# Kernel tuning notes

Hardware: AMD Instinct MI355X
Metric: run time of the kernel (lower is better)

The kernel has to match this reference:

```python
import jax, jax.numpy as jnp
import numpy as np

N = 4096        # nodes
E = 4096        # hyperedges (source math forces E == N)
B = 3           # behaviors
D_IN = 64
HID = 32
OUT = 32
L = 2           # num_layers
EPS = 1e-6      # DynamicPruningGNN.epsilon
DEG_P = 0.008   # ~32 incidences per node


def setup_inputs() -> dict:
    key = jax.random.key(0)
    ks = jax.random.split(key, 12)
    sc = lambda f: 1.0 / np.sqrt(f)
    X = jax.random.normal(ks[0], (N, D_IN), jnp.float32)
    # sparse binary incidence matrices, stored dense as the original does (H.toarray())
    H = (jax.random.uniform(ks[1], (B, N, E)) < DEG_P).astype(jnp.float32)
    return {
        "X": X,
        "H": H,
        "W_init": jax.random.normal(ks[2], (D_IN, HID), jnp.float32) * sc(D_IN),
        "b_init": jnp.zeros((HID,), jnp.float32),
        "W_node": jax.random.normal(ks[3], (L, HID, HID), jnp.float32) * sc(HID),
        "b_node": jnp.zeros((L, HID), jnp.float32),
        "Theta": jax.random.normal(ks[4], (B, HID, HID), jnp.float32) * sc(HID),
        "behavior_importance": jnp.ones((B,), jnp.float32),
        "Wp1": jax.random.normal(ks[5], (HID, HID), jnp.float32) * sc(HID),
        "bp1": jnp.zeros((HID,), jnp.float32),
        "Wp2": jax.random.normal(ks[6], (HID, OUT), jnp.float32) * sc(HID),
        "bp2": jnp.zeros((OUT,), jnp.float32),
    }


def reference(X, H, W_init, b_init, W_node, b_node, Theta,
              behavior_importance, Wp1, bp1, Wp2, bp2):
    # degree normalizers, clamped like np.maximum(deg, epsilon)
    dv = 1.0 / jnp.sqrt(jnp.maximum(H.sum(axis=2), EPS))   # [B, N]  Dv^-1/2
    de = 1.0 / jnp.maximum(H.sum(axis=1), EPS)             # [B, E]  De^-1
    w = jax.nn.softmax(behavior_importance)                # behavior weights

    x = jax.nn.relu(X @ W_init + b_init)                   # initial_transform  [N, HID]
    for l in range(L):
        xw = x @ W_node[l] + b_node[l]                     # node layer          [N, HID]
        y = dv[:, :, None] * xw[None, :, :]                # Dv^-1/2 . XW       [B, N, HID]
        z = jnp.einsum('bne,bnh->beh', H, y) * de[:, :, None]   # De^-1 H^T ...  [B, E, HID]
        u = jnp.einsum('bne,beh->bnh', H, z) * dv[:, :, None]   # Dv^-1/2 H ...  [B, N, HID]
        msg = jnp.einsum('bnh,bhk->bnk', u, Theta)         # per-behavior Theta [B, N, HID]
        x = jax.nn.relu(jnp.einsum('b,bnk->nk', w, msg))   # weighted multi-behavior agg
    # node_projection: Linear -> ReLU -> Linear
    node_emb = jax.nn.relu(x @ Wp1 + bp1) @ Wp2 + bp2      # [N, OUT]
    return node_emb
```

## Files before the change

kernel.cpp:

```cpp
#include <hip/hip_runtime.h>

#define NN 4096
#define EE 4096
#define BB 3
#define DIN 64
#define HID 32
#define MAXDEG 64
#define EPSF 1e-6f

typedef float nfloat4 __attribute__((ext_vector_type(4)));

__global__ __launch_bounds__(256) void build_all(
        const float* __restrict__ H, const float* __restrict__ X,
        const float* __restrict__ Wi, const float* __restrict__ bi,
        const float* __restrict__ Wn0, const float* __restrict__ bn0,
        int* __restrict__ rowcnt, float* __restrict__ dvinv,
        int* __restrict__ colcnt,
        unsigned short* __restrict__ csr16, unsigned short* __restrict__ csc16,
        float* __restrict__ xw0) {
    __shared__ int el[MAXDEG];
    __shared__ int scnt;
    __shared__ float sh[HID];
    const int bn = blockIdx.x, tid = threadIdx.x;
    const int b = bn >> 12, nrel = bn & (NN - 1);
    if (tid == 0) scnt = 0;
    __syncthreads();
    const nfloat4* row = (const nfloat4*)(H + (size_t)bn * EE);
    nfloat4 v[4];
#pragma unroll
    for (int i = 0; i < 4; i++)
        v[i] = __builtin_nontemporal_load(row + tid + i * 256);
#pragma unroll
    for (int i = 0; i < 4; i++) {
        const nfloat4 w = v[i];
        const int mm = (w.x != 0.f) + (w.y != 0.f) + (w.z != 0.f) + (w.w != 0.f);
        if (mm) {
            int base = atomicAdd(&scnt, mm);
            const int e0 = (tid + i * 256) * 4;
            if (w.x != 0.f) { if (base < MAXDEG) el[base] = e0;     base++; }
            if (w.y != 0.f) { if (base < MAXDEG) el[base] = e0 + 1; base++; }
            if (w.z != 0.f) { if (base < MAXDEG) el[base] = e0 + 2; base++; }
            if (w.w != 0.f) { if (base < MAXDEG) el[base] = e0 + 3; base++; }
        }
    }
    __syncthreads();
    const int cnt = scnt;
    const int m = min(cnt, MAXDEG);
    if (tid == 0) {
        rowcnt[bn] = cnt;
        dvinv[bn] = rsqrtf(fmaxf((float)cnt, EPSF));
    }
    if (tid < MAXDEG)
        csr16[(size_t)bn * MAXDEG + tid] = (tid < m) ? (unsigned short)el[tid] : 0;
    if (tid < m) {
        const int q = (b << 12) + el[tid];
        const int slot = atomicAdd(&colcnt[q], 1);
        if (slot < MAXDEG) csc16[(size_t)q * MAXDEG + slot] = (unsigned short)nrel;
    }
    if (b == 0 && tid < HID) {
        const int h = tid;
        const float* xr = X + (size_t)nrel * DIN;
        float acc = bi[h];
#pragma unroll 8
        for (int d = 0; d < DIN; d++) acc = fmaf(xr[d], Wi[d * HID + h], acc);
        sh[h] = fmaxf(acc, 0.f);
        float a = bn0[h];
#pragma unroll
        for (int k = 0; k < HID; k++) a = fmaf(sh[k], Wn0[k * HID + h], a);
        xw0[nrel * HID + h] = a;
    }
}

__global__ __launch_bounds__(256) void k_z(
        const int* __restrict__ colcnt, const unsigned short* __restrict__ csc16,
        const float* __restrict__ xw, const float* __restrict__ dvinv,
        float* __restrict__ zbuf) {
    const int tid = threadIdx.x, h = tid & 31, g = tid >> 5;
    const int q = blockIdx.x * 8 + g;
    const int cnt = colcnt[q];
    const int m = min(cnt, MAXDEG);
    const int dvbase = q & ~(NN - 1);
    const unsigned int packed = ((const unsigned int*)csc16)[q * 32 + h];
    float acc[8] = {0.f, 0.f, 0.f, 0.f, 0.f, 0.f, 0.f, 0.f};
    for (int j0 = 0; j0 < m; j0 += 8) {
        float vs[8];
#pragma unroll
        for (int k = 0; k < 8; k++) {
            const int j = j0 + k;
            const unsigned int p = __shfl(packed, j >> 1, 32);
            const int id = (j & 1) ? (int)(p >> 16) : (int)(p & 0xffffu);
            vs[k] = xw[id * HID + h] * dvinv[dvbase + id];
        }
#pragma unroll
        for (int k = 0; k < 8; k++) if (j0 + k < m) acc[k] += vs[k];
    }
    const float s = ((acc[0] + acc[1]) + (acc[2] + acc[3]))
                  + ((acc[4] + acc[5]) + (acc[6] + acc[7]));
    zbuf[(size_t)q * HID + h] = s * (1.0f / fmaxf((float)cnt, EPSF));
}

__device__ __forceinline__ float gatherz(const float* __restrict__ zb,
                                         unsigned int packed, int m, int h) {
    float acc[8] = {0.f, 0.f, 0.f, 0.f, 0.f, 0.f, 0.f, 0.f};
    for (int j0 = 0; j0 < m; j0 += 8) {
        float vs[8];
#pragma unroll
        for (int k = 0; k < 8; k++) {
            const int j = j0 + k;
            const unsigned int p = __shfl(packed, j >> 1, 32);
            const int id = (j & 1) ? (int)(p >> 16) : (int)(p & 0xffffu);
            vs[k] = zb[id * HID + h];
        }
#pragma unroll
        for (int k = 0; k < 8; k++) if (j0 + k < m) acc[k] += vs[k];
    }
    return ((acc[0] + acc[1]) + (acc[2] + acc[3]))
         + ((acc[4] + acc[5]) + (acc[6] + acc[7]));
}

__device__ __forceinline__ void softmax3(const float* __restrict__ bimp, float* sw) {
    float b0 = bimp[0], b1 = bimp[1], b2 = bimp[2];
    float mm = fmaxf(b0, fmaxf(b1, b2));
    float e0 = expf(b0 - mm), e1 = expf(b1 - mm), e2 = expf(b2 - mm);
    float s = e0 + e1 + e2;
    sw[0] = e0 / s; sw[1] = e1 / s; sw[2] = e2 / s;
}

__global__ __launch_bounds__(256) void k_layer(
        const float* __restrict__ zbuf,
        const int* __restrict__ rowcnt, const unsigned short* __restrict__ csr16,
        const float* __restrict__ Theta, const float* __restrict__ bimp,
        const float* __restrict__ Wn1, const float* __restrict__ bn1,
        float* __restrict__ xw1) {
    __shared__ float sTh[BB * HID * HID];
    __shared__ float sW[HID * HID];
    __shared__ float sb[HID];
    __shared__ float su[8][HID];
    __shared__ float sw[4];
    const int tid = threadIdx.x;
    for (int i = tid; i < BB * HID * HID; i += 256) sTh[i] = Theta[i];
    for (int i = tid; i < HID * HID; i += 256) sW[i] = Wn1[i];
    if (tid < HID) sb[tid] = bn1[tid];
    if (tid == 0) softmax3(bimp, sw);
    __syncthreads();
    const int h = tid & 31, loc = tid >> 5;
    const int n = blockIdx.x * 8 + loc;
    float accx = 0.f;
#pragma unroll
    for (int b = 0; b < BB; b++) {
        const int r = (b << 12) + n;
        const int cnt = rowcnt[r];
        const int m = min(cnt, MAXDEG);
        const unsigned int packed = ((const unsigned int*)csr16)[r * 32 + h];
        const float u = gatherz(zbuf + (size_t)(b << 12) * HID, packed, m, h)
                        * rsqrtf(fmaxf((float)cnt, EPSF));
        su[loc][h] = u;
        float msg = 0.f;
#pragma unroll
        for (int hh = 0; hh < HID; hh++)
            msg = fmaf(su[loc][hh], sTh[b * (HID * HID) + hh * HID + h], msg);
        accx = fmaf(sw[b], msg, accx);
    }
    su[loc][h] = fmaxf(accx, 0.f);
    float a = sb[h];
#pragma unroll
    for (int hh = 0; hh < HID; hh++) a = fmaf(su[loc][hh], sW[hh * HID + h], a);
    xw1[n * HID + h] = a;
}

__global__ __launch_bounds__(256) void k_final(
        const float* __restrict__ zbuf,
        const int* __restrict__ rowcnt, const unsigned short* __restrict__ csr16,
        const float* __restrict__ Theta, const float* __restrict__ bimp,
        const float* __restrict__ Wp1, const float* __restrict__ bp1,
        const float* __restrict__ Wp2, const float* __restrict__ bp2,
        float* __restrict__ out) {
    __shared__ float sTh[BB * HID * HID];
    __shared__ float sW1[HID * HID], sW2[HID * HID];
    __shared__ float sb1[HID], sb2[HID];
    __shared__ float su[8][HID];
    __shared__ float sw[4];
    const int tid = threadIdx.x;
    for (int i = tid; i < BB * HID * HID; i += 256) sTh[i] = Theta[i];
    for (int i = tid; i < HID * HID; i += 256) { sW1[i] = Wp1[i]; sW2[i] = Wp2[i]; }
    if (tid < HID) { sb1[tid] = bp1[tid]; sb2[tid] = bp2[tid]; }
    if (tid == 0) softmax3(bimp, sw);
    __syncthreads();
    const int h = tid & 31, loc = tid >> 5;
    const int n = blockIdx.x * 8 + loc;
    float accx = 0.f;
#pragma unroll
    for (int b = 0; b < BB; b++) {
        const int r = (b << 12) + n;
        const int cnt = rowcnt[r];
        const int m = min(cnt, MAXDEG);
        const unsigned int packed = ((const unsigned int*)csr16)[r * 32 + h];
        const float u = gatherz(zbuf + (size_t)(b << 12) * HID, packed, m, h)
                        * rsqrtf(fmaxf((float)cnt, EPSF));
        su[loc][h] = u;
        float msg = 0.f;
#pragma unroll
        for (int hh = 0; hh < HID; hh++)
            msg = fmaf(su[loc][hh], sTh[b * (HID * HID) + hh * HID + h], msg);
        accx = fmaf(sw[b], msg, accx);
    }
    su[loc][h] = fmaxf(accx, 0.f);
    float p = sb1[h];
#pragma unroll
    for (int hh = 0; hh < HID; hh++) p = fmaf(su[loc][hh], sW1[hh * HID + h], p);
    su[loc][h] = fmaxf(p, 0.f);
    float o = sb2[h];
#pragma unroll
    for (int hh = 0; hh < HID; hh++) o = fmaf(su[loc][hh], sW2[hh * HID + h], o);
    out[(size_t)n * HID + h] = o;
}

extern "C" void kernel_launch(void* const* d_in, const int* in_sizes, int n_in,
                              void* d_out, int out_size, void* d_ws, size_t ws_size,
                              hipStream_t stream) {
    const float* X      = (const float*)d_in[0];
    const float* H      = (const float*)d_in[1];
    const float* W_init = (const float*)d_in[2];
    const float* b_init = (const float*)d_in[3];
    const float* W_node = (const float*)d_in[4];
    const float* b_node = (const float*)d_in[5];
    const float* Theta  = (const float*)d_in[6];
    const float* bimp   = (const float*)d_in[7];
    const float* Wp1    = (const float*)d_in[8];
    const float* bp1    = (const float*)d_in[9];
    const float* Wp2    = (const float*)d_in[10];
    const float* bp2    = (const float*)d_in[11];
    float* out = (float*)d_out;
    (void)in_sizes; (void)n_in; (void)out_size; (void)ws_size;

    char* ws = (char*)d_ws;
    size_t off = 0;
    auto alloc = [&](size_t bytes) { void* p = ws + off; off += (bytes + 255) & ~(size_t)255; return p; };
    int*            rowcnt = (int*)alloc((size_t)BB * NN * 4);
    float*          dvinv  = (float*)alloc((size_t)BB * NN * 4);
    int*            colcnt = (int*)alloc((size_t)BB * EE * 4);
    unsigned short* csr16  = (unsigned short*)alloc((size_t)BB * NN * MAXDEG * 2);
    unsigned short* csc16  = (unsigned short*)alloc((size_t)BB * EE * MAXDEG * 2);
    float*          xw0    = (float*)alloc((size_t)NN * HID * 4);
    float*          xw1    = (float*)alloc((size_t)NN * HID * 4);
    float*          zbuf   = (float*)alloc((size_t)BB * EE * HID * 4);

    (void)hipMemsetAsync(colcnt, 0, (size_t)BB * EE * 4, stream);
    build_all<<<BB * NN, 256, 0, stream>>>(H, X, W_init, b_init, W_node, b_node,
                                           rowcnt, dvinv, colcnt, csr16, csc16, xw0);
    k_z<<<(BB * EE) / 8, 256, 0, stream>>>(colcnt, csc16, xw0, dvinv, zbuf);
    k_layer<<<NN / 8, 256, 0, stream>>>(zbuf, rowcnt, csr16, Theta, bimp,
                                        W_node + HID * HID, b_node + HID, xw1);
    k_z<<<(BB * EE) / 8, 256, 0, stream>>>(colcnt, csc16, xw1, dvinv, zbuf);
    k_final<<<NN / 8, 256, 0, stream>>>(zbuf, rowcnt, csr16, Theta, bimp,
                                        Wp1, bp1, Wp2, bp2, out);
}
```

Baseline: 335.0 us.

## Fuse all stages into one persistent kernel with software grid barriers

Replaces the five separate launches (build, two z-gathers, layer, final) with a single persistent kernel of 768 blocks that loops over work and separates phases with atomic-counter grid barriers. Barrier counters are zeroed together with colcnt in the existing memset. The aim is to remove launch gaps and tail effects between the small dependent kernels. The barrier relies on all 768 blocks being co-resident and has a spin timeout. The build phase now runs with fewer blocks, so it may lose some memory-level parallelism on the dense H scan.

Result: slower. 878.9 us (+162.3%).

```diff
diff --git a/kernel.cpp b/kernel.cpp
--- a/kernel.cpp
+++ b/kernel.cpp
@@ -7,96 +7,27 @@
 #define HID 32
 #define MAXDEG 64
 #define EPSF 1e-6f
+#define GRID 768
+#define ROWS (BB * NN)
 
 typedef float nfloat4 __attribute__((ext_vector_type(4)));
 
-__global__ __launch_bounds__(256) void build_all(
-        const float* __restrict__ H, const float* __restrict__ X,
-        const float* __restrict__ Wi, const float* __restrict__ bi,
-        const float* __restrict__ Wn0, const float* __restrict__ bn0,
-        int* __restrict__ rowcnt, float* __restrict__ dvinv,
-        int* __restrict__ colcnt,
-        unsigned short* __restrict__ csr16, unsigned short* __restrict__ csc16,
-        float* __restrict__ xw0) {
-    __shared__ int el[MAXDEG];
-    __shared__ int scnt;
-    __shared__ float sh[HID];
-    const int bn = blockIdx.x, tid = threadIdx.x;
-    const int b = bn >> 12, nrel = bn & (NN - 1);
-    if (tid == 0) scnt = 0;
+__device__ __forceinline__ void gridbar(int* __restrict__ barcnt, int idx) {
     __syncthreads();
-    const nfloat4* row = (const nfloat4*)(H + (size_t)bn * EE);
-    nfloat4 v[4];
-#pragma unroll
-    for (int i = 0; i < 4; i++)
-        v[i] = __builtin_nontemporal_load(row + tid + i * 256);
-#pragma unroll
-    for (int i = 0; i < 4; i++) {
-        const nfloat4 w = v[i];
-        const int mm = (w.x != 0.f) + (w.y != 0.f) + (w.z != 0.f) + (w.w != 0.f);
-        if (mm) {
-            int base = atomicAdd(&scnt, mm);
-            const int e0 = (tid + i * 256) * 4;
-            if (w.x != 0.f) { if (base < MAXDEG) el[base] = e0;     base++; }
-            if (w.y != 0.f) { if (base < MAXDEG) el[base] = e0 + 1; base++; }
-            if (w.z != 0.f) { if (base < MAXDEG) el[base] = e0 + 2; base++; }
-            if (w.w != 0.f) { if (base < MAXDEG) el[base] = e0 + 3; base++; }
-        }
+    if (threadIdx.x == 0) {
+        __threadfence();
+        __hip_atomic_fetch_add(barcnt + idx * 64, 1,
+                               __ATOMIC_RELEASE, __HIP_MEMORY_SCOPE_AGENT);
+        int spins = 0;
+        while (__hip_atomic_load(barcnt + idx * 64,
+                                 __ATOMIC_ACQUIRE, __HIP_MEMORY_SCOPE_AGENT) < GRID
+               && spins < (1 << 24)) {
+            __builtin_amdgcn_s_sleep(2);
+            ++spins;
+        }
+        __threadfence();
     }
     __syncthreads();
-    const int cnt = scnt;
-    const int m = min(cnt, MAXDEG);
-    if (tid == 0) {
-        rowcnt[bn] = cnt;
-        dvinv[bn] = rsqrtf(fmaxf((float)cnt, EPSF));
-    }
-    if (tid < MAXDEG)
-        csr16[(size_t)bn * MAXDEG + tid] = (tid < m) ? (unsigned short)el[tid] : 0;
-    if (tid < m) {
-        const int q = (b << 12) + el[tid];
-        const int slot = atomicAdd(&colcnt[q], 1);
-        if (slot < MAXDEG) csc16[(size_t)q * MAXDEG + slot] = (unsigned short)nrel;
-    }
-    if (b == 0 && tid < HID) {
-        const int h = tid;
-        const float* xr = X + (size_t)nrel * DIN;
-        float acc = bi[h];
-#pragma unroll 8
-        for (int d = 0; d < DIN; d++) acc = fmaf(xr[d], Wi[d * HID + h], acc);
-        sh[h] = fmaxf(acc, 0.f);
-        float a = bn0[h];
-#pragma unroll
-        for (int k = 0; k < HID; k++) a = fmaf(sh[k], Wn0[k * HID + h], a);
-        xw0[nrel * HID + h] = a;
-    }
-}
-
-__global__ __launch_bounds__(256) void k_z(
-        const int* __restrict__ colcnt, const unsigned short* __restrict__ csc16,
-        const float* __restrict__ xw, const float* __restrict__ dvinv,
-        float* __restrict__ zbuf) {
-    const int tid = threadIdx.x, h = tid & 31, g = tid >> 5;
-    const int q = blockIdx.x * 8 + g;
-    const int cnt = colcnt[q];
-    const int m = min(cnt, MAXDEG);
-    const int dvbase = q & ~(NN - 1);
-    const unsigned int packed = ((const unsigned int*)csc16)[q * 32 + h];
-    float acc[8] = {0.f, 0.f, 0.f, 0.f, 0.f, 0.f, 0.f, 0.f};
-    for (int j0 = 0; j0 < m; j0 += 8) {
-        float vs[8];
-#pragma unroll
-        for (int k = 0; k < 8; k++) {
-            const int j = j0 + k;
-            const unsigned int p = __shfl(packed, j >> 1, 32);
-            const int id = (j & 1) ? (int)(p >> 16) : (int)(p & 0xffffu);
-            vs[k] = xw[id * HID + h] * dvinv[dvbase + id];
-        }
-#pragma unroll
-        for (int k = 0; k < 8; k++) if (j0 + k < m) acc[k] += vs[k];
-    }
-    const float s = ((acc[0] + acc[1]) + (acc[2] + acc[3]))
-                  + ((acc[4] + acc[5]) + (acc[6] + acc[7]));
-    zbuf[(size_t)q * HID + h] = s * (1.0f / fmaxf((float)cnt, EPSF));
 }
 
 __device__ __forceinline__ float gatherz(const float* __restrict__ zb,
@@ -126,93 +57,193 @@
     sw[0] = e0 / s; sw[1] = e1 / s; sw[2] = e2 / s;
 }
 
-__global__ __launch_bounds__(256) void k_layer(
-        const float* __restrict__ zbuf,
-        const int* __restrict__ rowcnt, const unsigned short* __restrict__ csr16,
-        const float* __restrict__ Theta, const float* __restrict__ bimp,
+__global__ __launch_bounds__(256, 4) void mega(
+        const float* __restrict__ H, const float* __restrict__ X,
+        const float* __restrict__ Wi, const float* __restrict__ bi,
+        const float* __restrict__ Wn0, const float* __restrict__ bn0,
         const float* __restrict__ Wn1, const float* __restrict__ bn1,
-        float* __restrict__ xw1) {
-    __shared__ float sTh[BB * HID * HID];
-    __shared__ float sW[HID * HID];
-    __shared__ float sb[HID];
-    __shared__ float su[8][HID];
-    __shared__ float sw[4];
-    const int tid = threadIdx.x;
-    for (int i = tid; i < BB * HID * HID; i += 256) sTh[i] = Theta[i];
-    for (int i = tid; i < HID * HID; i += 256) sW[i] = Wn1[i];
-    if (tid < HID) sb[tid] = bn1[tid];
-    if (tid == 0) softmax3(bimp, sw);
-    __syncthreads();
-    const int h = tid & 31, loc = tid >> 5;
-    const int n = blockIdx.x * 8 + loc;
-    float accx = 0.f;
-#pragma unroll
-    for (int b = 0; b < BB; b++) {
-        const int r = (b << 12) + n;
-        const int cnt = rowcnt[r];
-        const int m = min(cnt, MAXDEG);
-        const unsigned int packed = ((const unsigned int*)csr16)[r * 32 + h];
-        const float u = gatherz(zbuf + (size_t)(b << 12) * HID, packed, m, h)
-                        * rsqrtf(fmaxf((float)cnt, EPSF));
-        su[loc][h] = u;
-        float msg = 0.f;
-#pragma unroll
-        for (int hh = 0; hh < HID; hh++)
-            msg = fmaf(su[loc][hh], sTh[b * (HID * HID) + hh * HID + h], msg);
-        accx = fmaf(sw[b], msg, accx);
-    }
-    su[loc][h] = fmaxf(accx, 0.f);
-    float a = sb[h];
-#pragma unroll
-    for (int hh = 0; hh < HID; hh++) a = fmaf(su[loc][hh], sW[hh * HID + h], a);
-    xw1[n * HID + h] = a;
-}
-
-__global__ __launch_bounds__(256) void k_final(
-        const float* __restrict__ zbuf,
-        const int* __restrict__ rowcnt, const unsigned short* __restrict__ csr16,
         const float* __restrict__ Theta, const float* __restrict__ bimp,
         const float* __restrict__ Wp1, const float* __restrict__ bp1,
         const float* __restrict__ Wp2, const float* __restrict__ bp2,
-        float* __restrict__ out) {
+        int* __restrict__ rowcnt, float* __restrict__ dvinv,
+        int* __restrict__ colcnt, unsigned short* __restrict__ csr16,
+        unsigned short* __restrict__ csc16, float* __restrict__ xw0,
+        float* __restrict__ xw1, float* __restrict__ zbuf,
+        int* barcnt, float* __restrict__ out) {
     __shared__ float sTh[BB * HID * HID];
     __shared__ float sW1[HID * HID], sW2[HID * HID];
     __shared__ float sb1[HID], sb2[HID];
     __shared__ float su[8][HID];
     __shared__ float sw[4];
-    const int tid = threadIdx.x;
-    for (int i = tid; i < BB * HID * HID; i += 256) sTh[i] = Theta[i];
-    for (int i = tid; i < HID * HID; i += 256) { sW1[i] = Wp1[i]; sW2[i] = Wp2[i]; }
-    if (tid < HID) { sb1[tid] = bp1[tid]; sb2[tid] = bp2[tid]; }
-    if (tid == 0) softmax3(bimp, sw);
-    __syncthreads();
-    const int h = tid & 31, loc = tid >> 5;
-    const int n = blockIdx.x * 8 + loc;
-    float accx = 0.f;
-#pragma unroll
-    for (int b = 0; b < BB; b++) {
-        const int r = (b << 12) + n;
-        const int cnt = rowcnt[r];
+    __shared__ int el[MAXDEG];
+    __shared__ int scnt;
+    __shared__ float sh[HID];
+
+    const int tid = threadIdx.x, bid = blockIdx.x;
+    const int h = tid & 31, w = tid >> 5;
+    const int gw = bid * 8 + w;
+
+    for (int bn = bid; bn < ROWS; bn += GRID) {
+        const int b = bn >> 12, nrel = bn & (NN - 1);
+        if (tid == 0) scnt = 0;
+        __syncthreads();
+        const nfloat4* row = (const nfloat4*)(H + (size_t)bn * EE);
+        nfloat4 v[4];
+#pragma unroll
+        for (int i = 0; i < 4; i++)
+            v[i] = __builtin_nontemporal_load(row + tid + i * 256);
+#pragma unroll
+        for (int i = 0; i < 4; i++) {
+            const nfloat4 vv = v[i];
+            const int mm = (vv.x != 0.f) + (vv.y != 0.f) + (vv.z != 0.f) + (vv.w != 0.f);
+            if (mm) {
+                int base = atomicAdd(&scnt, mm);
+                const int e0 = (tid + i * 256) * 4;
+                if (vv.x != 0.f) { if (base < MAXDEG) el[base] = e0;     base++; }
+                if (vv.y != 0.f) { if (base < MAXDEG) el[base] = e0 + 1; base++; }
+                if (vv.z != 0.f) { if (base < MAXDEG) el[base] = e0 + 2; base++; }
+                if (vv.w != 0.f) { if (base < MAXDEG) el[base] = e0 + 3; base++; }
+            }
+        }
+        __syncthreads();
+        const int cnt = scnt;
         const int m = min(cnt, MAXDEG);
-        const unsigned int packed = ((const unsigned int*)csr16)[r * 32 + h];
-        const float u = gatherz(zbuf + (size_t)(b << 12) * HID, packed, m, h)
-                        * rsqrtf(fmaxf((float)cnt, EPSF));
-        su[loc][h] = u;
-        float msg = 0.f;
-#pragma unroll
-        for (int hh = 0; hh < HID; hh++)
-            msg = fmaf(su[loc][hh], sTh[b * (HID * HID) + hh * HID + h], msg);
-        accx = fmaf(sw[b], msg, accx);
-    }
-    su[loc][h] = fmaxf(accx, 0.f);
-    float p = sb1[h];
-#pragma unroll
-    for (int hh = 0; hh < HID; hh++) p = fmaf(su[loc][hh], sW1[hh * HID + h], p);
-    su[loc][h] = fmaxf(p, 0.f);
-    float o = sb2[h];
-#pragma unroll
-    for (int hh = 0; hh < HID; hh++) o = fmaf(su[loc][hh], sW2[hh * HID + h], o);
-    out[(size_t)n * HID + h] = o;
+        if (tid == 0) {
+            rowcnt[bn] = cnt;
+            dvinv[bn] = rsqrtf(fmaxf((float)cnt, EPSF));
+        }
+        if (tid < MAXDEG)
+            csr16[(size_t)bn * MAXDEG + tid] = (tid < m) ? (unsigned short)el[tid] : 0;
+        if (tid < m) {
+            const int q = (b << 12) + el[tid];
+            const int slot = atomicAdd(&colcnt[q], 1);
+            if (slot < MAXDEG) csc16[(size_t)q * MAXDEG + slot] = (unsigned short)nrel;
+        }
+        if (b == 0 && tid < HID) {
+            const float* xr = X + (size_t)nrel * DIN;
+            float acc = bi[tid];
+#pragma unroll 8
+            for (int d = 0; d < DIN; d++) acc = fmaf(xr[d], Wi[d * HID + tid], acc);
+            sh[tid] = fmaxf(acc, 0.f);
+            float a = bn0[tid];
+#pragma unroll
+            for (int k = 0; k < HID; k++) a = fmaf(sh[k], Wn0[k * HID + tid], a);
+            xw0[nrel * HID + tid] = a;
+        }
+        __syncthreads();
+    }
+    gridbar(barcnt, 0);
+
+    for (int q = gw; q < ROWS; q += GRID * 8) {
+        const int cnt = colcnt[q];
+        const int m = min(cnt, MAXDEG);
+        const int dvbase = q & ~(NN - 1);
+        const unsigned int packed = ((const unsigned int*)csc16)[q * 32 + h];
+        float acc[8] = {0.f, 0.f, 0.f, 0.f, 0.f, 0.f, 0.f, 0.f};
+        for (int j0 = 0; j0 < m; j0 += 8) {
+            float vs[8];
+#pragma unroll
+            for (int k = 0; k < 8; k++) {
+                const int j = j0 + k;
+                const unsigned int p = __shfl(packed, j >> 1, 32);
+                const int id = (j & 1) ? (int)(p >> 16) : (int)(p & 0xffffu);
+                vs[k] = xw0[id * HID + h] * dvinv[dvbase + id];
+            }
+#pragma unroll
+            for (int k = 0; k < 8; k++) if (j0 + k < m) acc[k] += vs[k];
+        }
+        const float s = ((acc[0] + acc[1]) + (acc[2] + acc[3]))
+                      + ((acc[4] + acc[5]) + (acc[6] + acc[7]));
+        zbuf[(size_t)q * HID + h] = s * (1.0f / fmaxf((float)cnt, EPSF));
+    }
+    gridbar(barcnt, 1);
+
+    if (bid < NN / 8) {
+        for (int i = tid; i < BB * HID * HID; i += 256) sTh[i] = Theta[i];
+        for (int i = tid; i < HID * HID; i += 256) sW1[i] = Wn1[i];
+        if (tid < HID) sb1[tid] = bn1[tid];
+        if (tid == 0) softmax3(bimp, sw);
+        __syncthreads();
+        const int n = gw;
+        float accx = 0.f;
+#pragma unroll
+        for (int b = 0; b < BB; b++) {
+            const int r = (b << 12) + n;
+            const int cnt = rowcnt[r];
+            const int m = min(cnt, MAXDEG);
+            const unsigned int packed = ((const unsigned int*)csr16)[r * 32 + h];
+            const float u = gatherz(zbuf + (size_t)(b << 12) * HID, packed, m, h)
+                            * rsqrtf(fmaxf((float)cnt, EPSF));
+            su[w][h] = u;
+            float msg = 0.f;
+#pragma unroll
+            for (int hh = 0; hh < HID; hh++)
+                msg = fmaf(su[w][hh], sTh[b * (HID * HID) + hh * HID + h], msg);
+            accx = fmaf(sw[b], msg, accx);
+        }
+        su[w][h] = fmaxf(accx, 0.f);
+        float a = sb1[h];
+#pragma unroll
+        for (int hh = 0; hh < HID; hh++) a = fmaf(su[w][hh], sW1[hh * HID + h], a);
+        xw1[n * HID + h] = a;
+    }
+    gridbar(barcnt, 2);
+
+    for (int q = gw; q < ROWS; q += GRID * 8) {
+        const int cnt = colcnt[q];
+        const int m = min(cnt, MAXDEG);
+        const int dvbase = q & ~(NN - 1);
+        const unsigned int packed = ((const unsigned int*)csc16)[q * 32 + h];
+        float acc[8] = {0.f, 0.f, 0.f, 0.f, 0.f, 0.f, 0.f, 0.f};
+        for (int j0 = 0; j0 < m; j0 += 8) {
+            float vs[8];
+#pragma unroll
+            for (int k = 0; k < 8; k++) {
+                const int j = j0 + k;
+                const unsigned int p = __shfl(packed, j >> 1, 32);
+                const int id = (j & 1) ? (int)(p >> 16) : (int)(p & 0xffffu);
+                vs[k] = xw1[id * HID + h] * dvinv[dvbase + id];
+            }
+#pragma unroll
+            for (int k = 0; k < 8; k++) if (j0 + k < m) acc[k] += vs[k];
+        }
+        const float s = ((acc[0] + acc[1]) + (acc[2] + acc[3]))
+                      + ((acc[4] + acc[5]) + (acc[6] + acc[7]));
+        zbuf[(size_t)q * HID + h] = s * (1.0f / fmaxf((float)cnt, EPSF));
+    }
+    gridbar(barcnt, 3);
+
+    if (bid < NN / 8) {
+        for (int i = tid; i < HID * HID; i += 256) { sW1[i] = Wp1[i]; sW2[i] = Wp2[i]; }
+        if (tid < HID) { sb1[tid] = bp1[tid]; sb2[tid] = bp2[tid]; }
+        __syncthreads();
+        const int n = gw;
+        float accx = 0.f;
+#pragma unroll
+        for (int b = 0; b < BB; b++) {
+            const int r = (b << 12) + n;
+            const int cnt = rowcnt[r];
+            const int m = min(cnt, MAXDEG);
+            const unsigned int packed = ((const unsigned int*)csr16)[r * 32 + h];
+            const float u = gatherz(zbuf + (size_t)(b << 12) * HID, packed, m, h)
+                            * rsqrtf(fmaxf((float)cnt, EPSF));
+            su[w][h] = u;
+            float msg = 0.f;
+#pragma unroll
+            for (int hh = 0; hh < HID; hh++)
+                msg = fmaf(su[w][hh], sTh[b * (HID * HID) + hh * HID + h], msg);
+            accx = fmaf(sw[b], msg, accx);
+        }
+        su[w][h] = fmaxf(accx, 0.f);
+        float p = sb1[h];
+#pragma unroll
+        for (int hh = 0; hh < HID; hh++) p = fmaf(su[w][hh], sW1[hh * HID + h], p);
+        su[w][h] = fmaxf(p, 0.f);
+        float o = sb2[h];
+#pragma unroll
+        for (int hh = 0; hh < HID; hh++) o = fmaf(su[w][hh], sW2[hh * HID + h], o);
+        out[(size_t)n * HID + h] = o;
+    }
 }
 
 extern "C" void kernel_launch(void* const* d_in, const int* in_sizes, int n_in,
@@ -239,19 +270,17 @@
     int*            rowcnt = (int*)alloc((size_t)BB * NN * 4);
     float*          dvinv  = (float*)alloc((size_t)BB * NN * 4);
     int*            colcnt = (int*)alloc((size_t)BB * EE * 4);
+    int*            barcnt = (int*)alloc(4 * 64 * 4);
     unsigned short* csr16  = (unsigned short*)alloc((size_t)BB * NN * MAXDEG * 2);
     unsigned short* csc16  = (unsigned short*)alloc((size_t)BB * EE * MAXDEG * 2);
     float*          xw0    = (float*)alloc((size_t)NN * HID * 4);
     float*          xw1    = (float*)alloc((size_t)NN * HID * 4);
     float*          zbuf   = (float*)alloc((size_t)BB * EE * HID * 4);
 
-    (void)hipMemsetAsync(colcnt, 0, (size_t)BB * EE * 4, stream);
-    build_all<<<BB * NN, 256, 0, stream>>>(H, X, W_init, b_init, W_node, b_node,
-                                           rowcnt, dvinv, colcnt, csr16, csc16, xw0);
-    k_z<<<(BB * EE) / 8, 256, 0, stream>>>(colcnt, csc16, xw0, dvinv, zbuf);
-    k_layer<<<NN / 8, 256, 0, stream>>>(zbuf, rowcnt, csr16, Theta, bimp,
-                                        W_node + HID * HID, b_node + HID, xw1);
-    k_z<<<(BB * EE) / 8, 256, 0, stream>>>(colcnt, csc16, xw1, dvinv, zbuf);
-    k_final<<<NN / 8, 256, 0, stream>>>(zbuf, rowcnt, csr16, Theta, bimp,
-                                        Wp1, bp1, Wp2, bp2, out);
-}
+    (void)hipMemsetAsync(colcnt, 0, (size_t)BB * EE * 4 + 4 * 64 * 4, stream);
+    mega<<<GRID, 256, 0, stream>>>(H, X, W_init, b_init,
+                                   W_node, b_node, W_node + HID * HID, b_node + HID,
+                                   Theta, bimp, Wp1, bp1, Wp2, bp2,
+                                   rowcnt, dvinv, colcnt, csr16, csc16,
+                                   xw0, xw1, zbuf, barcnt, out);
+}
```
